# Kernel tuning notes

Hardware: AMD Instinct MI355X
Metric: run time of the kernel (lower is better)

## Reference

```python
import jax, jax.numpy as jnp
import numpy as np

N, E, H, NOISE, T, G = 50000, 400000, 128, 64, 128, 16
EPS = 1e-5


def _graph_norm(x, seg, num_seg, w, b, ms):
    # PyG GraphNorm: per-graph mean/std with learnable mean_scale
    cnt = jnp.maximum(jax.ops.segment_sum(jnp.ones((x.shape[0],), x.dtype), seg, num_segments=num_seg), 1.0)
    mean = jax.ops.segment_sum(x, seg, num_segments=num_seg) / cnt[:, None]
    out = x - mean[seg] * ms
    var = jax.ops.segment_sum(out * out, seg, num_segments=num_seg) / cnt[:, None]
    return w * out / jnp.sqrt(var + EPS)[seg] + b


def _forward(features, noise_mapping_emb, time_emb,
             We, be, Wp, bp, Wq, bq, Wr, br, Wu, bu, Wv, bv,
             gnh_w, gnh_b, gnh_ms, gne_w, gne_b, gne_ms,
             Wt, bt, ln_w, ln_b, Wo, bo,
             edge_mapping_idx, batch):
    src, dst = edge_mapping_idx[0], edge_mapping_idx[1]
    nme = noise_mapping_emb @ We + be                                  # [E,H]
    e_hat = nme @ Wp + bp + (features @ Wq + bq)[src] + (features @ Wr + br)[dst]
    gates = jax.nn.sigmoid(e_hat)
    aggr = jax.ops.segment_sum((features @ Wv + bv)[dst] * gates, src, num_segments=N)
    h = _graph_norm(features @ Wu + bu + aggr, batch, G, gnh_w, gnh_b, gnh_ms)
    eseg = batch[src]                                                  # edge -> graph
    e = _graph_norm(e_hat, eseg, G, gne_w, gne_b, gne_ms)
    h = jax.nn.relu(h)
    e = jax.nn.relu(e)
    e = e + (jax.nn.relu(time_emb) @ Wt + bt)[eseg]
    h = features + h
    # out_layer: LayerNorm -> SiLU -> Linear
    mu = jnp.mean(e, axis=-1, keepdims=True)
    var = jnp.mean((e - mu) ** 2, axis=-1, keepdims=True)
    ln = (e - mu) / jnp.sqrt(var + EPS) * ln_w + ln_b
    e = nme + jax.nn.silu(ln) @ Wo + bo
    return h, e


def setup_inputs() -> dict:
    key = jax.random.key(0)
    ks = jax.random.split(key, 16)

    def lin(k, i, o):
        k1, k2 = jax.random.split(k)
        s = 1.0 / np.sqrt(i)
        return (jax.random.uniform(k1, (i, o), minval=-s, maxval=s, dtype=jnp.float32),
                jax.random.uniform(k2, (o,), minval=-s, maxval=s, dtype=jnp.float32))

    We, be = lin(ks[5], NOISE, H)
    Wp, bp = lin(ks[6], H, H)
    Wq, bq = lin(ks[7], H, H)
    Wr, br = lin(ks[8], H, H)
    Wu, bu = lin(ks[9], H, H)
    Wv, bv = lin(ks[10], H, H)
    Wt, bt = lin(ks[11], T, H)
    Wo, bo = lin(ks[12], H, H)
    ones = jnp.ones((H,), jnp.float32)
    zeros = jnp.zeros((H,), jnp.float32)
    return dict(
        features=jax.random.normal(ks[0], (N, H), dtype=jnp.float32),
        edge_mapping_idx=jax.random.randint(ks[1], (2, E), 0, N),
        noise_mapping_emb=jax.random.normal(ks[2], (E, NOISE), dtype=jnp.float32),
        time_emb=jax.random.normal(ks[3], (G, T), dtype=jnp.float32),
        batch=jnp.sort(jax.random.randint(ks[4], (N,), 0, G)),
        We=We, be=be, Wp=Wp, bp=bp, Wq=Wq, bq=bq, Wr=Wr, br=br,
        Wu=Wu, bu=bu, Wv=Wv, bv=bv,
        gnh_w=ones, gnh_b=zeros, gnh_ms=ones,
        gne_w=ones, gne_b=zeros, gne_ms=ones,
        Wt=Wt, bt=bt, ln_w=ones, ln_b=zeros, Wo=Wo, bo=bo,
    )


def reference(features, edge_mapping_idx, noise_mapping_emb, time_emb, batch,
              We, be, Wp, bp, Wq, bq, Wr, br, Wu, bu, Wv, bv,
              gnh_w, gnh_b, gnh_ms, gne_w, gne_b, gne_ms,
              Wt, bt, ln_w, ln_b, Wo, bo):
    return _forward(features, noise_mapping_emb, time_emb,
                    We, be, Wp, bp, Wq, bq, Wr, br, Wu, bu, Wv, bv,
                    gnh_w, gnh_b, gnh_ms, gne_w, gne_b, gne_ms,
                    Wt, bt, ln_w, ln_b, Wo, bo,
                    edge_mapping_idx, batch)
```

## Files before the change

### kernel.cpp

```cpp
#include <hip/hip_runtime.h>

#define NN 50000
#define NE 400000
#define HD 128
#define ND 64
#define GG 16
#define EPSV 1e-5f
#define ETILE 64

#define SLEN (2 * GG * HD + GG)
#define PSTRIDE 4352
#define EP 512
#define HP 256
#define AGB 2048

typedef unsigned short u16;
typedef unsigned int   u32;
typedef unsigned char  u8;
typedef __attribute__((__ext_vector_type__(8))) __bf16 bf16x8;
typedef __attribute__((__ext_vector_type__(4))) float  f32x4;

__device__ __forceinline__ float us2f(u16 u) { return __uint_as_float(((u32)u) << 16); }
__device__ __forceinline__ u16 f2us(float f) {
    u32 u = __float_as_uint(f);
    u += 0x7fffu + ((u >> 16) & 1u);
    return (u16)(u >> 16);
}
__device__ __forceinline__ float sigmoidf_(float x) { return 1.f / (1.f + __expf(-x)); }

__global__ __launch_bounds__(256) void wep_kernel(
    const float* __restrict__ We, const float* __restrict__ Wp,
    const float* __restrict__ be, const float* __restrict__ bp,
    float* __restrict__ Wep, float* __restrict__ bep)
{
    __shared__ float wp[HD][HD];
    const int t = threadIdx.x;
    for (int i = t; i < HD * HD; i += 256) wp[i >> 7][i & 127] = Wp[i];
    __syncthreads();
    const int c = t & 127;
    for (int r = blockIdx.x * 4 + (t >> 7); r < (blockIdx.x + 1) * 4 && r < ND; r += 2) {
        float a = 0.f;
        for (int k = 0; k < HD; ++k) a = fmaf(We[r * HD + k], wp[k][c], a);
        Wep[r * HD + c] = a;
    }
    if (blockIdx.x == 0 && t < HD) {
        float a = bp[t];
        for (int k = 0; k < HD; ++k) a = fmaf(be[k], wp[k][t], a);
        bep[t] = a;
    }
}

__global__ __launch_bounds__(256) void prep_all_kernel(
    const float* __restrict__ Wq, const float* __restrict__ Wr,
    const float* __restrict__ Wv, const float* __restrict__ Wu,
    const float* __restrict__ Wo, const float* __restrict__ Wep,
    const float* __restrict__ We,
    u16* __restrict__ WqT, u16* __restrict__ WrT, u16* __restrict__ WvT,
    u16* __restrict__ WuT, u16* __restrict__ WoT, u16* __restrict__ WepT,
    u16* __restrict__ WeT)
{
    const float* in; u16* out; int K;
    switch (blockIdx.y) {
        case 0: in = Wq;  out = WqT;  K = HD; break;
        case 1: in = Wr;  out = WrT;  K = HD; break;
        case 2: in = Wv;  out = WvT;  K = HD; break;
        case 3: in = Wu;  out = WuT;  K = HD; break;
        case 4: in = Wo;  out = WoT;  K = HD; break;
        case 5: in = Wep; out = WepT; K = ND; break;
        default: in = We; out = WeT;  K = ND; break;
    }
    int idx = blockIdx.x * 256 + threadIdx.x;
    if (idx >= K * HD) return;
    int k = idx >> 7, n = idx & 127;
    out[n * K + k] = f2us(in[idx]);
}

__global__ __launch_bounds__(256) void hist_kernel(
    const int* __restrict__ srcArr, u32* __restrict__ deg)
{
    int e = blockIdx.x * 256 + threadIdx.x;
    if (e >= NE) return;
    atomicAdd(&deg[srcArr[e]], 1u);
}

#define SCAN_C 49
__global__ __launch_bounds__(1024) void scan_kernel(
    const u32* __restrict__ deg, int* __restrict__ start)
{
    __shared__ u32 sums[1024];
    const int t = threadIdx.x;
    const int i0 = t * SCAN_C;
    u32 tot = 0;
    for (int j = 0; j < SCAN_C; ++j) { int i = i0 + j; if (i < NN) tot += deg[i]; }
    sums[t] = tot;
    __syncthreads();
    for (int off = 1; off < 1024; off <<= 1) {
        u32 v = (t >= off) ? sums[t - off] : 0u;
        __syncthreads();
        sums[t] += v;
        __syncthreads();
    }
    u32 run = (t == 0) ? 0u : sums[t - 1];
    for (int j = 0; j < SCAN_C; ++j) {
        int i = i0 + j;
        if (i < NN) { start[i] = (int)run; run += deg[i]; }
    }
    if (t == 1023) start[NN] = (int)run;
}

__global__ __launch_bounds__(256) void scatter_kernel(
    const int* __restrict__ srcArr, const int* __restrict__ dstArr,
    const int* __restrict__ batch, const int* __restrict__ start,
    u32* __restrict__ cnt2, int* __restrict__ perm,
    int* __restrict__ iperm,
    int* __restrict__ src_csr, int* __restrict__ dst_csr,
    u8* __restrict__ g8csr)
{
    int e = blockIdx.x * 256 + threadIdx.x;
    if (e >= NE) return;
    int s = srcArr[e];
    u32 pos = atomicAdd(&cnt2[s], 1u);
    int j = start[s] + (int)pos;
    perm[j] = e;
    iperm[e] = j;
    src_csr[j] = s;
    dst_csr[j] = dstArr[e];
    g8csr[j] = (u8)batch[s];
}

__global__ __launch_bounds__(256) void proj4_kernel(
    const float* __restrict__ feat,
    const u16* __restrict__ WqT, const u16* __restrict__ WrT,
    const u16* __restrict__ WvT, const u16* __restrict__ WuT,
    const float* __restrict__ bq, const float* __restrict__ br,
    const float* __restrict__ bv, const float* __restrict__ bu,
    u16* __restrict__ fq, u16* __restrict__ fr, u16* __restrict__ fv,
    float* __restrict__ fu32)
{
    __shared__ __align__(16) u16 As[ETILE * HD];
    const int t = threadIdx.x;
    const int rbase = blockIdx.x * ETILE;
    #pragma unroll
    for (int i = 0; i < 16; ++i) {
        int idx2 = t + i * 256;
        int row = idx2 >> 6, p = idx2 & 63;
        int grow = rbase + row;
        float2 v = make_float2(0.f, 0.f);
        if (grow < NN) v = *reinterpret_cast<const float2*>(&feat[(size_t)grow * HD + p * 2]);
        u32 pk = (u32)f2us(v.x) | ((u32)f2us(v.y) << 16);
        int off = (row * 256 + p * 4) ^ ((row & 7) << 4);
        *reinterpret_cast<u32*>(reinterpret_cast<char*>(As) + off) = pk;
    }
    __syncthreads();
    const int w = t >> 6, lane = t & 63;
    const int rt = w * 16, l15 = lane & 15, kg = lane >> 4;
    const int lrow = rt + l15;
    bf16x8 afr[4];
    #pragma unroll
    for (int kk = 0; kk < 4; ++kk) {
        int off = (lrow * 256 + (kk * 32 + kg * 8) * 2) ^ ((lrow & 7) << 4);
        afr[kk] = *reinterpret_cast<const bf16x8*>(reinterpret_cast<const char*>(As) + off);
    }
    const u16* WTs[4] = {WqT, WrT, WvT, WuT};
    const float* Bs2[4] = {bq, br, bv, bu};
    u16* Os[3] = {fq, fr, fv};
    #pragma unroll
    for (int m = 0; m < 4; ++m) {
        f32x4 acc[8];
        #pragma unroll
        for (int nt = 0; nt < 8; ++nt) { acc[nt][0]=0.f; acc[nt][1]=0.f; acc[nt][2]=0.f; acc[nt][3]=0.f; }
        const u16* W = WTs[m];
        #pragma unroll
        for (int nt = 0; nt < 8; ++nt) {
            #pragma unroll
            for (int kk = 0; kk < 4; ++kk) {
                bf16x8 b = *reinterpret_cast<const bf16x8*>(&W[(nt * 16 + l15) * HD + kk * 32 + kg * 8]);
                acc[nt] = __builtin_amdgcn_mfma_f32_16x16x32_bf16(afr[kk], b, acc[nt], 0, 0, 0);
            }
        }
        #pragma unroll
        for (int nt = 0; nt < 8; ++nt) {
            int gcol = nt * 16 + l15;
            float bias = Bs2[m][gcol];
            #pragma unroll
            for (int i = 0; i < 4; ++i) {
                int grow = rbase + rt + kg * 4 + i;
                if (grow < NN) {
                    float v = acc[nt][i] + bias;
                    if (m < 3) Os[m][(size_t)grow * HD + gcol] = f2us(v);
                    else       fu32[(size_t)grow * HD + gcol] = v;
                }
            }
        }
    }
}

__global__ __launch_bounds__(256) void ehat_kernel(
    const float* __restrict__ noise, const u16* __restrict__ WepT,
    const float* __restrict__ bep,
    const u16* __restrict__ fq, const u16* __restrict__ fr,
    const int* __restrict__ perm, const int* __restrict__ src_csr,
    const int* __restrict__ dst_csr,
    u16* __restrict__ ehat_csr)
{
    __shared__ __align__(16) u16 WeL[1024 * 8];
    const int t = threadIdx.x;
    #pragma unroll
    for (int q = 0; q < 4; ++q) {
        int f = t + q * 256;
        int fl15 = f & 15, kgi = (f >> 4) & 7, fnt = f >> 7;
        *reinterpret_cast<uint4*>(&WeL[f * 8]) =
            *reinterpret_cast<const uint4*>(&WepT[(size_t)(fnt * 16 + fl15) * ND + kgi * 8]);
    }
    const int rbase = blockIdx.x * ETILE;
    const int w = t >> 6, lane = t & 63;
    const int rt = w * 16, l15 = lane & 15, kg = lane >> 4;
    const int jl = rbase + rt + l15;
    const int el = perm[jl];
    u32 an[2][4];
    #pragma unroll
    for (int kk = 0; kk < 2; ++kk) {
        const int c = kk * 32 + kg * 8;
        float4 n0 = *reinterpret_cast<const float4*>(&noise[(size_t)el * ND + c]);
        float4 n1 = *reinterpret_cast<const float4*>(&noise[(size_t)el * ND + c + 4]);
        an[kk][0] = (u32)f2us(n0.x) | ((u32)f2us(n0.y) << 16);
        an[kk][1] = (u32)f2us(n0.z) | ((u32)f2us(n0.w) << 16);
        an[kk][2] = (u32)f2us(n1.x) | ((u32)f2us(n1.y) << 16);
        an[kk][3] = (u32)f2us(n1.z) | ((u32)f2us(n1.w) << 16);
    }
    __syncthreads();
    f32x4 acc[8];
    #pragma unroll
    for (int nt = 0; nt < 8; ++nt) {
        float b = bep[nt * 16 + l15];
        acc[nt][0] = b; acc[nt][1] = b; acc[nt][2] = b; acc[nt][3] = b;
    }
    const int lid = kg * 16 + l15;
    #pragma unroll
    for (int nt = 0; nt < 8; ++nt) {
        #pragma unroll
        for (int kk = 0; kk < 2; ++kk) {
            bf16x8 b = *reinterpret_cast<const bf16x8*>(&WeL[(((nt * 2 + kk) * 64) + lid) * 8]);
            acc[nt] = __builtin_amdgcn_mfma_f32_16x16x32_bf16(
                *reinterpret_cast<const bf16x8*>(an[kk]), b, acc[nt], 0, 0, 0);
        }
    }
    #pragma unroll
    for (int i = 0; i < 4; ++i) {
        int jrow = rbase + rt + kg * 4 + i;
        int s = src_csr[jrow], d = dst_csr[jrow];
        #pragma unroll
        for (int nt = 0; nt < 8; ++nt) {
            int gcol = nt * 16 + l15;
            float v = acc[nt][i]
                    + us2f(fq[(size_t)s * HD + gcol]) + us2f(fr[(size_t)d * HD + gcol]);
            ehat_csr[(size_t)jrow * HD + gcol] = f2us(v);
        }
    }
}

__global__ __launch_bounds__(256) void aggr_kernel(
    const u16* __restrict__ ehat_csr, const u16* __restrict__ fv,
    const int* __restrict__ dst_csr, const int* __restrict__ start,
    float* __restrict__ xout)
{
    const int wid = blockIdx.x * 4 + (threadIdx.x >> 6);
    const int lane = threadIdx.x & 63;
    const int c0 = lane * 2;
    const int NW = AGB * 4;
    const int chunk = (NN + NW - 1) / NW;
    const int n0 = wid * chunk;
    const int n1 = min(NN, n0 + chunk);
    for (int node = n0; node < n1; ++node) {
        int s0 = start[node], s1 = start[node + 1];
        float2 uv = *reinterpret_cast<const float2*>(&xout[(size_t)node * HD + c0]);
        float a0 = 0.f, a1 = 0.f;
        for (int j = s0; j < s1; ++j) {
            int d = dst_csr[j];
            u32 ev = *reinterpret_cast<const u32*>(&ehat_csr[(size_t)j * HD + c0]);
            u32 vv = *reinterpret_cast<const u32*>(&fv[(size_t)d * HD + c0]);
            a0 = fmaf(sigmoidf_(us2f((u16)ev)),         us2f((u16)vv),         a0);
            a1 = fmaf(sigmoidf_(us2f((u16)(ev >> 16))), us2f((u16)(vv >> 16)), a1);
        }
        *reinterpret_cast<float2*>(&xout[(size_t)node * HD + c0]) =
            make_float2(a0 + uv.x, a1 + uv.y);
    }
}

__global__ __launch_bounds__(256) void hstats_part_kernel(
    const float* __restrict__ xout, const int* __restrict__ batch,
    float* __restrict__ hpart)
{
    __shared__ float sm[SLEN];
    const int t = threadIdx.x;
    for (int i = t; i < SLEN; i += 256) sm[i] = 0.f;
    __syncthreads();
    const int cg = t & 15, rq = t >> 4;
    const int c8 = cg * 8;
    const int chunk = (NN + HP - 1) / HP;
    const int rstart = blockIdx.x * chunk;
    const int rend = min(NN, rstart + chunk);
    float s0[8], z0[8];
    #pragma unroll
    for (int p = 0; p < 8; ++p) { s0[p] = 0.f; z0[p] = 0.f; }
    float cn = 0.f;
    int curg = -1;
    for (int row = rstart + rq; row < rend; row += 16) {
        int g = batch[row];
        if (g != curg) {
            if (curg >= 0) {
                #pragma unroll
                for (int p = 0; p < 8; ++p) {
                    unsafeAtomicAdd(&sm[curg * HD + c8 + p], s0[p]);
                    unsafeAtomicAdd(&sm[2048 + curg * HD + c8 + p], z0[p]);
                    s0[p] = 0.f; z0[p] = 0.f;
                }
                if (cg == 0) { unsafeAtomicAdd(&sm[4096 + curg], cn); }
                cn = 0.f;
            }
            curg = g;
        }
        float4 xa = *reinterpret_cast<const float4*>(&xout[(size_t)row * HD + c8]);
        float4 xb = *reinterpret_cast<const float4*>(&xout[(size_t)row * HD + c8 + 4]);
        const float xs8[8] = {xa.x, xa.y, xa.z, xa.w, xb.x, xb.y, xb.z, xb.w};
        #pragma unroll
        for (int p = 0; p < 8; ++p) { s0[p] += xs8[p]; z0[p] = fmaf(xs8[p], xs8[p], z0[p]); }
        cn += (cg == 0) ? 1.f : 0.f;
    }
    if (curg >= 0) {
        #pragma unroll
        for (int p = 0; p < 8; ++p) {
            unsafeAtomicAdd(&sm[curg * HD + c8 + p], s0[p]);
            unsafeAtomicAdd(&sm[2048 + curg * HD + c8 + p], z0[p]);
        }
        if (cg == 0) { unsafeAtomicAdd(&sm[4096 + curg], cn); }
    }
    __syncthreads();
    float* dst = hpart + (size_t)blockIdx.x * PSTRIDE;
    for (int i = t; i < SLEN; i += 256) dst[i] = sm[i];
}

__global__ __launch_bounds__(512) void estats_part_kernel(
    const u16* __restrict__ ehat_csr, const u8* __restrict__ g8csr,
    float* __restrict__ epart)
{
    __shared__ float sm[SLEN];
    const int t = threadIdx.x;
    for (int i = t; i < SLEN; i += 512) sm[i] = 0.f;
    __syncthreads();
    const int cg = t & 15, rq = t >> 4;
    const int c8 = cg * 8;
    const int chunk = (NE + EP - 1) / EP;
    const int rstart = blockIdx.x * chunk;
    const int rend = min(NE, rstart + chunk);
    float s0[8], z0[8];
    #pragma unroll
    for (int p = 0; p < 8; ++p) { s0[p] = 0.f; z0[p] = 0.f; }
    float cn = 0.f;
    int curg = -1;
    for (int row = rstart + rq; row < rend; row += 32) {
        int g = (int)g8csr[row];
        if (g != curg) {
            if (curg >= 0) {
                #pragma unroll
                for (int p = 0; p < 8; ++p) {
                    unsafeAtomicAdd(&sm[curg * HD + c8 + p], s0[p]);
                    unsafeAtomicAdd(&sm[2048 + curg * HD + c8 + p], z0[p]);
                    s0[p] = 0.f; z0[p] = 0.f;
                }
                if (cg == 0) { unsafeAtomicAdd(&sm[4096 + curg], cn); }
                cn = 0.f;
            }
            curg = g;
        }
        uint4 ev = *reinterpret_cast<const uint4*>(&ehat_csr[(size_t)row * HD + c8]);
        const u32 wds[4] = {ev.x, ev.y, ev.z, ev.w};
        #pragma unroll
        for (int p2 = 0; p2 < 4; ++p2) {
            float x0 = us2f((u16)wds[p2]);
            float x1 = us2f((u16)(wds[p2] >> 16));
            s0[2 * p2]     += x0; z0[2 * p2]     = fmaf(x0, x0, z0[2 * p2]);
            s0[2 * p2 + 1] += x1; z0[2 * p2 + 1] = fmaf(x1, x1, z0[2 * p2 + 1]);
        }
        cn += (cg == 0) ? 1.f : 0.f;
    }
    if (curg >= 0) {
        #pragma unroll
        for (int p = 0; p < 8; ++p) {
            unsafeAtomicAdd(&sm[curg * HD + c8 + p], s0[p]);
            unsafeAtomicAdd(&sm[2048 + curg * HD + c8 + p], z0[p]);
        }
        if (cg == 0) { unsafeAtomicAdd(&sm[4096 + curg], cn); }
    }
    __syncthreads();
    float* dst = epart + (size_t)blockIdx.x * PSTRIDE;
    for (int i = t; i < SLEN; i += 512) dst[i] = sm[i];
}

__global__ __launch_bounds__(256) void reduce_part_kernel(
    const float* __restrict__ part, int P, int csz, float* __restrict__ out)
{
    int j = blockIdx.x * 256 + threadIdx.x;
    if (j >= SLEN) return;
    int p0 = blockIdx.y * csz;
    int p1 = min(P, p0 + csz);
    float a = 0.f;
    for (int p = p0; p < p1; ++p) a += part[(size_t)p * PSTRIDE + j];
    out[(size_t)blockIdx.y * PSTRIDE + j] = a;
}

__global__ __launch_bounds__(256) void finstats_kernel(
    const float* __restrict__ statsH, const float* __restrict__ statsE,
    const float* __restrict__ gnh_ms, const float* __restrict__ gne_ms,
    const float* __restrict__ gnh_w, const float* __restrict__ gnh_b,
    const float* __restrict__ gne_w, const float* __restrict__ gne_b,
    const float* __restrict__ ln_w, const float* __restrict__ ln_b,
    const float* __restrict__ be, const float* __restrict__ bo,
    float* __restrict__ SBh, float* __restrict__ SBe,
    float* __restrict__ LNWB, float* __restrict__ bsum)
{
    const int t = threadIdx.x;
    if (t < 64) {
        LNWB[4 * t]     = ln_w[2 * t];
        LNWB[4 * t + 1] = ln_b[2 * t];
        LNWB[4 * t + 2] = ln_w[2 * t + 1];
        LNWB[4 * t + 3] = ln_b[2 * t + 1];
    }
    if (t >= 64 && t < 192) bsum[t - 64] = be[t - 64] + bo[t - 64];
    for (int i = t; i < GG * HD; i += 256) {
        int g = i >> 7, c = i & 127;
        {
            float cnt = fmaxf(statsH[4096 + g], 1.f);
            float mean = statsH[i] / cnt;
            float ex2 = statsH[2048 + i] / cnt;
            float off = mean * gnh_ms[c];
            float var = ex2 - 2.f * off * mean + off * off;
            float S = gnh_w[c] * rsqrtf(var + EPSV);
            SBh[2 * i]     = S;
            SBh[2 * i + 1] = gnh_b[c] - off * S;
        }
        {
            float cnt = fmaxf(statsE[4096 + g], 1.f);
            float mean = statsE[i] / cnt;
            float ex2 = statsE[2048 + i] / cnt;
            float off = mean * gne_ms[c];
            float var = ex2 - 2.f * off * mean + off * off;
            float S = gne_w[c] * rsqrtf(var + EPSV);
            SBe[2 * i]     = S;
            SBe[2 * i + 1] = gne_b[c] - off * S;
        }
    }
}

__global__ __launch_bounds__(256) void tproj_kernel(
    const float* __restrict__ time_emb, const float* __restrict__ Wt,
    const float* __restrict__ bt, float* __restrict__ tproj)
{
    __shared__ float te[GG][HD];
    const int t = threadIdx.x;
    for (int i = t; i < GG * HD; i += 256) te[i >> 7][i & 127] = fmaxf(time_emb[i], 0.f);
    __syncthreads();
    const int c = t & 127, rb = t >> 7;
    float acc[8];
    #pragma unroll
    for (int j = 0; j < 8; ++j) acc[j] = 0.f;
    for (int k = 0; k < HD; ++k) {
        float wv = Wt[k * HD + c];
        #pragma unroll
        for (int j = 0; j < 8; ++j) acc[j] = fmaf(te[rb + 2 * j][k], wv, acc[j]);
    }
    float b = bt[c];
    #pragma unroll
    for (int j = 0; j < 8; ++j) tproj[(rb + 2 * j) * HD + c] = acc[j] + b;
}

__global__ __launch_bounds__(256) void hfinal_kernel(
    const float* __restrict__ feat, const int* __restrict__ batch,
    const float* __restrict__ SBh, float* hout_x)
{
    int i = blockIdx.x * 256 + threadIdx.x;
    size_t base = (size_t)i * 4;
    if (base >= (size_t)NN * HD) return;
    int row = (int)(base >> 7), c0 = (int)(base & 127);
    int g = batch[row];
    float4 fe = *reinterpret_cast<const float4*>(&feat[base]);
    float4 xv = *reinterpret_cast<const float4*>(&hout_x[base]);
    float4 sb0 = *reinterpret_cast<const float4*>(&SBh[(size_t)(g * HD + c0) * 2]);
    float4 sb1 = *reinterpret_cast<const float4*>(&SBh[(size_t)(g * HD + c0 + 2) * 2]);
    float4 ou;
    ou.x = fe.x + fmaxf(fmaf(xv.x, sb0.x, sb0.y), 0.f);
    ou.y = fe.y + fmaxf(fmaf(xv.y, sb0.z, sb0.w), 0.f);
    ou.z = fe.z + fmaxf(fmaf(xv.z, sb1.x, sb1.y), 0.f);
    ou.w = fe.w + fmaxf(fmaf(xv.w, sb1.z, sb1.w), 0.f);
    *reinterpret_cast<float4*>(&hout_x[base]) = ou;
}

__global__ __launch_bounds__(256) void eprep_kernel(
    u16* __restrict__ ehat_csr, const u8* __restrict__ g8csr,
    const float* __restrict__ SBe, const float* __restrict__ tproj,
    const float* __restrict__ LNWB)
{
    const int t = threadIdx.x;
    const int lane = t & 63;
    const int cl = (lane & 15) * 8;
    const int wrow = (t >> 6) * 4 + (lane >> 4);
    for (int j = blockIdx.x * 16 + wrow; j < NE; j += gridDim.x * 16) {
        int g = g8csr[j];
        uint4 ev = *reinterpret_cast<const uint4*>(&ehat_csr[(size_t)j * HD + cl]);
        const u32 wds[4] = {ev.x, ev.y, ev.z, ev.w};
        float v[8];
        float lsum = 0.f;
        #pragma unroll
        for (int p = 0; p < 4; ++p) {
            int c2 = cl + p * 2;
            float x0 = us2f((u16)wds[p]);
            float x1 = us2f((u16)(wds[p] >> 16));
            float4 sb = *reinterpret_cast<const float4*>(&SBe[(size_t)(g * HD + c2) * 2]);
            float2 tp = *reinterpret_cast<const float2*>(&tproj[g * HD + c2]);
            float a0 = fmaxf(fmaf(x0, sb.x, sb.y), 0.f) + tp.x;
            float a1 = fmaxf(fmaf(x1, sb.z, sb.w), 0.f) + tp.y;
            v[p * 2] = a0; v[p * 2 + 1] = a1;
            lsum += a0 + a1;
        }
        lsum += __shfl_xor(lsum, 1, 64);
        lsum += __shfl_xor(lsum, 2, 64);
        lsum += __shfl_xor(lsum, 4, 64);
        lsum += __shfl_xor(lsum, 8, 64);
        float mu = lsum * (1.f / 128.f);
        float sq = 0.f;
        #pragma unroll
        for (int p = 0; p < 8; ++p) { float d = v[p] - mu; sq = fmaf(d, d, sq); }
        sq += __shfl_xor(sq, 1, 64);
        sq += __shfl_xor(sq, 2, 64);
        sq += __shfl_xor(sq, 4, 64);
        sq += __shfl_xor(sq, 8, 64);
        float rstd = rsqrtf(sq * (1.f / 128.f) + EPSV);
        u32 ow[4];
        #pragma unroll
        for (int p = 0; p < 4; ++p) {
            float4 lnwb = *reinterpret_cast<const float4*>(&LNWB[((cl >> 1) + p) * 4]);
            float l0 = (v[p * 2]     - mu) * rstd * lnwb.x + lnwb.y;
            float l1 = (v[p * 2 + 1] - mu) * rstd * lnwb.z + lnwb.w;
            float s0 = l0 * sigmoidf_(l0);
            float s1 = l1 * sigmoidf_(l1);
            ow[p] = (u32)f2us(s0) | ((u32)f2us(s1) << 16);
        }
        *reinterpret_cast<uint4*>(&ehat_csr[(size_t)j * HD + cl]) =
            make_uint4(ow[0], ow[1], ow[2], ow[3]);
    }
}

__global__ __launch_bounds__(512) void efinal_kernel(
    const u16* __restrict__ asilu, const float* __restrict__ noise,
    const int* __restrict__ iperm,
    const u16* __restrict__ WoT, const u16* __restrict__ WeT,
    const float* __restrict__ bsum,
    float* __restrict__ eout)
{
    __shared__ __align__(16) u16 WoL[2048 * 8];
    __shared__ __align__(16) u16 WeL[1024 * 8];
    const int t = threadIdx.x;
    #pragma unroll
    for (int q = 0; q < 4; ++q) {
        int f = t + q * 512;
        int l15 = f & 15, kgi = (f >> 4) & 15, nt = f >> 8;
        *reinterpret_cast<uint4*>(&WoL[f * 8]) =
            *reinterpret_cast<const uint4*>(&WoT[(size_t)(nt * 16 + l15) * HD + kgi * 8]);
    }
    #pragma unroll
    for (int q = 0; q < 2; ++q) {
        int f = t + q * 512;
        int l15 = f & 15, kgi = (f >> 4) & 7, nt = f >> 7;
        *reinterpret_cast<uint4*>(&WeL[f * 8]) =
            *reinterpret_cast<const uint4*>(&WeT[(size_t)(nt * 16 + l15) * ND + kgi * 8]);
    }

    const int rbase = blockIdx.x * 128;
    const int w = t >> 6, lane = t & 63;
    const int l15 = lane & 15, kg = lane >> 4;
    const int rt = w * 16;
    const int el = rbase + rt + l15;
    const int jl = iperm[el];

    bf16x8 aw[4];
    #pragma unroll
    for (int kk = 0; kk < 4; ++kk)
        aw[kk] = *reinterpret_cast<const bf16x8*>(&asilu[(size_t)jl * HD + kk * 32 + kg * 8]);
    u32 an[2][4];
    #pragma unroll
    for (int kk = 0; kk < 2; ++kk) {
        const int c = kk * 32 + kg * 8;
        float4 n0 = *reinterpret_cast<const float4*>(&noise[(size_t)el * ND + c]);
        float4 n1 = *reinterpret_cast<const float4*>(&noise[(size_t)el * ND + c + 4]);
        an[kk][0] = (u32)f2us(n0.x) | ((u32)f2us(n0.y) << 16);
        an[kk][1] = (u32)f2us(n0.z) | ((u32)f2us(n0.w) << 16);
        an[kk][2] = (u32)f2us(n1.x) | ((u32)f2us(n1.y) << 16);
        an[kk][3] = (u32)f2us(n1.z) | ((u32)f2us(n1.w) << 16);
    }
    __syncthreads();

    f32x4 acc[8];
    #pragma unroll
    for (int nt = 0; nt < 8; ++nt) {
        float bs = bsum[nt * 16 + l15];
        acc[nt][0] = bs; acc[nt][1] = bs; acc[nt][2] = bs; acc[nt][3] = bs;
    }
    const int lid = kg * 16 + l15;
    #pragma unroll
    for (int nt = 0; nt < 8; ++nt) {
        #pragma unroll
        for (int kk = 0; kk < 4; ++kk) {
            bf16x8 b = *reinterpret_cast<const bf16x8*>(&WoL[(((nt * 4 + kk) * 64) + lid) * 8]);
            acc[nt] = __builtin_amdgcn_mfma_f32_16x16x32_bf16(aw[kk], b, acc[nt], 0, 0, 0);
        }
        #pragma unroll
        for (int kk = 0; kk < 2; ++kk) {
            bf16x8 b = *reinterpret_cast<const bf16x8*>(&WeL[(((nt * 2 + kk) * 64) + lid) * 8]);
            acc[nt] = __builtin_amdgcn_mfma_f32_16x16x32_bf16(
                *reinterpret_cast<const bf16x8*>(an[kk]), b, acc[nt], 0, 0, 0);
        }
    }
    #pragma unroll
    for (int nt = 0; nt < 8; ++nt) {
        int gcol = nt * 16 + l15;
        #pragma unroll
        for (int i = 0; i < 4; ++i) {
            eout[(size_t)(rbase + rt + kg * 4 + i) * HD + gcol] = acc[nt][i];
        }
    }
}

extern "C" void kernel_launch(void* const* d_in, const int* in_sizes, int n_in,
                              void* d_out, int out_size, void* d_ws, size_t ws_size,
                              hipStream_t stream)
{
    const float* feat     = (const float*)d_in[0];
    const int*   eidx     = (const int*)d_in[1];
    const float* noise    = (const float*)d_in[2];
    const float* time_emb = (const float*)d_in[3];
    const int*   batch    = (const int*)d_in[4];
    const float* We = (const float*)d_in[5],  *be = (const float*)d_in[6];
    const float* Wp = (const float*)d_in[7],  *bp = (const float*)d_in[8];
    const float* Wq = (const float*)d_in[9],  *bq = (const float*)d_in[10];
    const float* Wr = (const float*)d_in[11], *br = (const float*)d_in[12];
    const float* Wu = (const float*)d_in[13], *bu = (const float*)d_in[14];
    const float* Wv = (const float*)d_in[15], *bv = (const float*)d_in[16];
    const float* gnh_w = (const float*)d_in[17], *gnh_b = (const float*)d_in[18], *gnh_ms = (const float*)d_in[19];
    const float* gne_w = (const float*)d_in[20], *gne_b = (const float*)d_in[21], *gne_ms = (const float*)d_in[22];
    const float* Wt = (const float*)d_in[23], *bt = (const float*)d_in[24];
    const float* ln_w = (const float*)d_in[25], *ln_b = (const float*)d_in[26];
    const float* Wo = (const float*)d_in[27], *bo = (const float*)d_in[28];

    const int* srcArr = eidx;
    const int* dstArr = eidx + NE;

    float* hout = (float*)d_out;
    float* eout = hout + (size_t)NN * HD;

    char* ws = (char*)d_ws;
    size_t off = 0;
    auto take = [&](size_t bytes) -> char* {
        char* p = ws + off;
        off = (off + bytes + 255) & ~(size_t)255;
        return p;
    };
    u16* ehat = (u16*)take((size_t)NE * HD * 2);
    u16* fq = (u16*)take((size_t)NN * HD * 2);
    u16* fr = (u16*)take((size_t)NN * HD * 2);
    u16* fv = (u16*)take((size_t)NN * HD * 2);
    u8*  g8csr = (u8*)take((size_t)NE);
    u32* deg  = (u32*)take((size_t)2 * NN * 4);
    u32* cnt2 = deg + NN;
    int* start = (int*)take((size_t)(NN + 1) * 4);
    int* perm  = (int*)take((size_t)NE * 4);
    int* iperm = (int*)take((size_t)NE * 4);
    int* src_csr = (int*)take((size_t)NE * 4);
    int* dst_csr = (int*)take((size_t)NE * 4);
    float* Wep = (float*)take((size_t)ND * HD * 4);
    float* bep = (float*)take((size_t)HD * 4);
    u16* WqT = (u16*)take((size_t)HD * HD * 2);
    u16* WrT = (u16*)take((size_t)HD * HD * 2);
    u16* WvT = (u16*)take((size_t)HD * HD * 2);
    u16* WuT = (u16*)take((size_t)HD * HD * 2);
    u16* WoT = (u16*)take((size_t)HD * HD * 2);
    u16* WepT = (u16*)take((size_t)HD * ND * 2);
    u16* WeT  = (u16*)take((size_t)HD * ND * 2);
    float* statsH = (float*)take((size_t)PSTRIDE * 4);
    float* statsE = (float*)take((size_t)PSTRIDE * 4);
    float* tproj  = (float*)take((size_t)GG * HD * 4);
    float* SBh    = (float*)take((size_t)GG * HD * 8);
    float* SBe    = (float*)take((size_t)GG * HD * 8);
    float* LNWB   = (float*)take((size_t)64 * 4 * 4);
    float* bsum   = (float*)take((size_t)HD * 4);
    float* epart  = (float*)take((size_t)EP * PSTRIDE * 4);
    float* hpart  = (float*)take((size_t)HP * PSTRIDE * 4);
    float* etmp   = (float*)take((size_t)8 * PSTRIDE * 4);
    float* htmp   = (float*)take((size_t)8 * PSTRIDE * 4);

    hipMemsetAsync(deg, 0, (size_t)2 * NN * 4, stream);

    wep_kernel<<<16, 256, 0, stream>>>(We, Wp, be, bp, Wep, bep);
    prep_all_kernel<<<dim3(64, 7), 256, 0, stream>>>(Wq, Wr, Wv, Wu, Wo, Wep, We,
                                                     WqT, WrT, WvT, WuT, WoT, WepT, WeT);
    hist_kernel<<<(NE + 255) / 256, 256, 0, stream>>>(srcArr, deg);
    scan_kernel<<<1, 1024, 0, stream>>>(deg, start);
    scatter_kernel<<<(NE + 255) / 256, 256, 0, stream>>>(srcArr, dstArr, batch, start,
                                                         cnt2, perm, iperm,
                                                         src_csr, dst_csr, g8csr);
    proj4_kernel<<<(NN + ETILE - 1) / ETILE, 256, 0, stream>>>(
        feat, WqT, WrT, WvT, WuT, bq, br, bv, bu, fq, fr, fv, hout);
    ehat_kernel<<<NE / ETILE, 256, 0, stream>>>(noise, WepT, bep, fq, fr,
                                                perm, src_csr, dst_csr, ehat);
    aggr_kernel<<<AGB, 256, 0, stream>>>(ehat, fv, dst_csr, start, hout);
    hstats_part_kernel<<<HP, 256, 0, stream>>>(hout, batch, hpart);
    estats_part_kernel<<<EP, 512, 0, stream>>>(ehat, g8csr, epart);
    {
        dim3 gA((SLEN + 255) / 256, 8);
        reduce_part_kernel<<<gA, 256, 0, stream>>>(hpart, HP, HP / 8, htmp);
        reduce_part_kernel<<<gA, 256, 0, stream>>>(epart, EP, EP / 8, etmp);
        dim3 gB((SLEN + 255) / 256, 1);
        reduce_part_kernel<<<gB, 256, 0, stream>>>(htmp, 8, 8, statsH);
        reduce_part_kernel<<<gB, 256, 0, stream>>>(etmp, 8, 8, statsE);
    }
    tproj_kernel<<<1, 256, 0, stream>>>(time_emb, Wt, bt, tproj);
    finstats_kernel<<<1, 256, 0, stream>>>(statsH, statsE, gnh_ms, gne_ms,
                                           gnh_w, gnh_b, gne_w, gne_b,
                                           ln_w, ln_b, be, bo,
                                           SBh, SBe, LNWB, bsum);
    eprep_kernel<<<2048, 256, 0, stream>>>(ehat, g8csr, SBe, tproj, LNWB);
    hfinal_kernel<<<(NN * HD / 4 + 255) / 256, 256, 0, stream>>>(feat, batch, SBh, hout);
    efinal_kernel<<<NE / 128, 512, 0, stream>>>(ehat, noise, iperm, WoT, WeT, bsum, eout);
}
```

Measured before the change: 692.0 us.

## Fuse node and edge GraphNorm statistics into the aggregation kernel

The aggregation kernel now also accumulates per-graph sum, sum-of-squares and count statistics for both the edge pre-activations and the aggregated node outputs, using shared-memory atomics on graph changes. This removes the two separate stats kernels, which each re-read ehat (E x H bf16) and the node output buffer. The cost is fewer blocks (512 x 512 threads) with more registers and shared memory in the aggregation pass, plus lower parallelism for the edge stats, which now follow the node-sharded CSR traversal. Edge graph ids come from batch[node], which is valid because edges are sorted by src.

Result: faster. 667.0 us (-3.6%).

```diff
diff --git a/kernel.cpp b/kernel.cpp
--- a/kernel.cpp
+++ b/kernel.cpp
@@ -10,9 +10,7 @@
 
 #define SLEN (2 * GG * HD + GG)
 #define PSTRIDE 4352
-#define EP 512
-#define HP 256
-#define AGB 2048
+#define ASB 512
 
 typedef unsigned short u16;
 typedef unsigned int   u32;
@@ -259,19 +257,48 @@
     }
 }
 
-__global__ __launch_bounds__(256) void aggr_kernel(
+__global__ __launch_bounds__(512) void aggr_stats_kernel(
     const u16* __restrict__ ehat_csr, const u16* __restrict__ fv,
     const int* __restrict__ dst_csr, const int* __restrict__ start,
-    float* __restrict__ xout)
-{
-    const int wid = blockIdx.x * 4 + (threadIdx.x >> 6);
-    const int lane = threadIdx.x & 63;
+    const int* __restrict__ batch, float* __restrict__ xout,
+    float* __restrict__ part)
+{
+    __shared__ float sm[2 * SLEN];
+    const int t = threadIdx.x;
+    for (int i = t; i < 2 * SLEN; i += 512) sm[i] = 0.f;
+    __syncthreads();
+    const int wid = blockIdx.x * 8 + (t >> 6);
+    const int lane = t & 63;
     const int c0 = lane * 2;
-    const int NW = AGB * 4;
+    const int NW = ASB * 8;
     const int chunk = (NN + NW - 1) / NW;
     const int n0 = wid * chunk;
     const int n1 = min(NN, n0 + chunk);
+    const float inc = (lane == 0) ? 1.f : 0.f;
+    float es0=0.f, es1=0.f, ez0=0.f, ez1=0.f, ecn=0.f;
+    float hs0=0.f, hs1=0.f, hz0=0.f, hz1=0.f, hcn=0.f;
+    int curg = -1;
     for (int node = n0; node < n1; ++node) {
+        int g = __builtin_amdgcn_readfirstlane(batch[node]);
+        if (g != curg) {
+            if (curg >= 0) {
+                unsafeAtomicAdd(&sm[curg * HD + c0],            es0);
+                unsafeAtomicAdd(&sm[curg * HD + c0 + 1],        es1);
+                unsafeAtomicAdd(&sm[2048 + curg * HD + c0],     ez0);
+                unsafeAtomicAdd(&sm[2048 + curg * HD + c0 + 1], ez1);
+                unsafeAtomicAdd(&sm[SLEN + curg * HD + c0],            hs0);
+                unsafeAtomicAdd(&sm[SLEN + curg * HD + c0 + 1],        hs1);
+                unsafeAtomicAdd(&sm[SLEN + 2048 + curg * HD + c0],     hz0);
+                unsafeAtomicAdd(&sm[SLEN + 2048 + curg * HD + c0 + 1], hz1);
+                if (lane == 0) {
+                    unsafeAtomicAdd(&sm[4096 + curg], ecn);
+                    unsafeAtomicAdd(&sm[SLEN + 4096 + curg], hcn);
+                }
+                es0=0.f; es1=0.f; ez0=0.f; ez1=0.f; ecn=0.f;
+                hs0=0.f; hs1=0.f; hz0=0.f; hz1=0.f; hcn=0.f;
+            }
+            curg = g;
+        }
         int s0 = start[node], s1 = start[node + 1];
         float2 uv = *reinterpret_cast<const float2*>(&xout[(size_t)node * HD + c0]);
         float a0 = 0.f, a1 = 0.f;
@@ -279,133 +306,51 @@
             int d = dst_csr[j];
             u32 ev = *reinterpret_cast<const u32*>(&ehat_csr[(size_t)j * HD + c0]);
             u32 vv = *reinterpret_cast<const u32*>(&fv[(size_t)d * HD + c0]);
-            a0 = fmaf(sigmoidf_(us2f((u16)ev)),         us2f((u16)vv),         a0);
-            a1 = fmaf(sigmoidf_(us2f((u16)(ev >> 16))), us2f((u16)(vv >> 16)), a1);
-        }
-        *reinterpret_cast<float2*>(&xout[(size_t)node * HD + c0]) =
-            make_float2(a0 + uv.x, a1 + uv.y);
-    }
-}
-
-__global__ __launch_bounds__(256) void hstats_part_kernel(
-    const float* __restrict__ xout, const int* __restrict__ batch,
-    float* __restrict__ hpart)
-{
-    __shared__ float sm[SLEN];
-    const int t = threadIdx.x;
-    for (int i = t; i < SLEN; i += 256) sm[i] = 0.f;
-    __syncthreads();
-    const int cg = t & 15, rq = t >> 4;
-    const int c8 = cg * 8;
-    const int chunk = (NN + HP - 1) / HP;
-    const int rstart = blockIdx.x * chunk;
-    const int rend = min(NN, rstart + chunk);
-    float s0[8], z0[8];
-    #pragma unroll
-    for (int p = 0; p < 8; ++p) { s0[p] = 0.f; z0[p] = 0.f; }
-    float cn = 0.f;
-    int curg = -1;
-    for (int row = rstart + rq; row < rend; row += 16) {
-        int g = batch[row];
-        if (g != curg) {
-            if (curg >= 0) {
-                #pragma unroll
-                for (int p = 0; p < 8; ++p) {
-                    unsafeAtomicAdd(&sm[curg * HD + c8 + p], s0[p]);
-                    unsafeAtomicAdd(&sm[2048 + curg * HD + c8 + p], z0[p]);
-                    s0[p] = 0.f; z0[p] = 0.f;
-                }
-                if (cg == 0) { unsafeAtomicAdd(&sm[4096 + curg], cn); }
-                cn = 0.f;
-            }
-            curg = g;
-        }
-        float4 xa = *reinterpret_cast<const float4*>(&xout[(size_t)row * HD + c8]);
-        float4 xb = *reinterpret_cast<const float4*>(&xout[(size_t)row * HD + c8 + 4]);
-        const float xs8[8] = {xa.x, xa.y, xa.z, xa.w, xb.x, xb.y, xb.z, xb.w};
-        #pragma unroll
-        for (int p = 0; p < 8; ++p) { s0[p] += xs8[p]; z0[p] = fmaf(xs8[p], xs8[p], z0[p]); }
-        cn += (cg == 0) ? 1.f : 0.f;
+            float x0 = us2f((u16)ev), x1 = us2f((u16)(ev >> 16));
+            a0 = fmaf(sigmoidf_(x0), us2f((u16)vv),         a0);
+            a1 = fmaf(sigmoidf_(x1), us2f((u16)(vv >> 16)), a1);
+            es0 += x0; ez0 = fmaf(x0, x0, ez0);
+            es1 += x1; ez1 = fmaf(x1, x1, ez1);
+            ecn += inc;
+        }
+        float xx0 = a0 + uv.x, xx1 = a1 + uv.y;
+        *reinterpret_cast<float2*>(&xout[(size_t)node * HD + c0]) = make_float2(xx0, xx1);
+        hs0 += xx0; hz0 = fmaf(xx0, xx0, hz0);
+        hs1 += xx1; hz1 = fmaf(xx1, xx1, hz1);
+        hcn += inc;
     }
     if (curg >= 0) {
-        #pragma unroll
-        for (int p = 0; p < 8; ++p) {
-            unsafeAtomicAdd(&sm[curg * HD + c8 + p], s0[p]);
-            unsafeAtomicAdd(&sm[2048 + curg * HD + c8 + p], z0[p]);
-        }
-        if (cg == 0) { unsafeAtomicAdd(&sm[4096 + curg], cn); }
-    }
-    __syncthreads();
-    float* dst = hpart + (size_t)blockIdx.x * PSTRIDE;
-    for (int i = t; i < SLEN; i += 256) dst[i] = sm[i];
-}
-
-__global__ __launch_bounds__(512) void estats_part_kernel(
-    const u16* __restrict__ ehat_csr, const u8* __restrict__ g8csr,
-    float* __restrict__ epart)
-{
-    __shared__ float sm[SLEN];
-    const int t = threadIdx.x;
-    for (int i = t; i < SLEN; i += 512) sm[i] = 0.f;
-    __syncthreads();
-    const int cg = t & 15, rq = t >> 4;
-    const int c8 = cg * 8;
-    const int chunk = (NE + EP - 1) / EP;
-    const int rstart = blockIdx.x * chunk;
-    const int rend = min(NE, rstart + chunk);
-    float s0[8], z0[8];
-    #pragma unroll
-    for (int p = 0; p < 8; ++p) { s0[p] = 0.f; z0[p] = 0.f; }
-    float cn = 0.f;
-    int curg = -1;
-    for (int row = rstart + rq; row < rend; row += 32) {
-        int g = (int)g8csr[row];
-        if (g != curg) {
-            if (curg >= 0) {
-                #pragma unroll
-                for (int p = 0; p < 8; ++p) {
-                    unsafeAtomicAdd(&sm[curg * HD + c8 + p], s0[p]);
-                    unsafeAtomicAdd(&sm[2048 + curg * HD + c8 + p], z0[p]);
-                    s0[p] = 0.f; z0[p] = 0.f;
-                }
-                if (cg == 0) { unsafeAtomicAdd(&sm[4096 + curg], cn); }
-                cn = 0.f;
-            }
-            curg = g;
-        }
-        uint4 ev = *reinterpret_cast<const uint4*>(&ehat_csr[(size_t)row * HD + c8]);
-        const u32 wds[4] = {ev.x, ev.y, ev.z, ev.w};
-        #pragma unroll
-        for (int p2 = 0; p2 < 4; ++p2) {
-            float x0 = us2f((u16)wds[p2]);
-            float x1 = us2f((u16)(wds[p2] >> 16));
-            s0[2 * p2]     += x0; z0[2 * p2]     = fmaf(x0, x0, z0[2 * p2]);
-            s0[2 * p2 + 1] += x1; z0[2 * p2 + 1] = fmaf(x1, x1, z0[2 * p2 + 1]);
-        }
-        cn += (cg == 0) ? 1.f : 0.f;
-    }
-    if (curg >= 0) {
-        #pragma unroll
-        for (int p = 0; p < 8; ++p) {
-            unsafeAtomicAdd(&sm[curg * HD + c8 + p], s0[p]);
-            unsafeAtomicAdd(&sm[2048 + curg * HD + c8 + p], z0[p]);
-        }
-        if (cg == 0) { unsafeAtomicAdd(&sm[4096 + curg], cn); }
-    }
-    __syncthreads();
-    float* dst = epart + (size_t)blockIdx.x * PSTRIDE;
-    for (int i = t; i < SLEN; i += 512) dst[i] = sm[i];
+        unsafeAtomicAdd(&sm[curg * HD + c0],            es0);
+        unsafeAtomicAdd(&sm[curg * HD + c0 + 1],        es1);
+        unsafeAtomicAdd(&sm[2048 + curg * HD + c0],     ez0);
+        unsafeAtomicAdd(&sm[2048 + curg * HD + c0 + 1], ez1);
+        unsafeAtomicAdd(&sm[SLEN + curg * HD + c0],            hs0);
+        unsafeAtomicAdd(&sm[SLEN + curg * HD + c0 + 1],        hs1);
+        unsafeAtomicAdd(&sm[SLEN + 2048 + curg * HD + c0],     hz0);
+        unsafeAtomicAdd(&sm[SLEN + 2048 + curg * HD + c0 + 1], hz1);
+        if (lane == 0) {
+            unsafeAtomicAdd(&sm[4096 + curg], ecn);
+            unsafeAtomicAdd(&sm[SLEN + 4096 + curg], hcn);
+        }
+    }
+    __syncthreads();
+    float* dst = part + (size_t)blockIdx.x * (2 * PSTRIDE);
+    for (int i = t; i < SLEN; i += 512) {
+        dst[i] = sm[i];
+        dst[PSTRIDE + i] = sm[SLEN + i];
+    }
 }
 
 __global__ __launch_bounds__(256) void reduce_part_kernel(
-    const float* __restrict__ part, int P, int csz, float* __restrict__ out)
+    const float* __restrict__ part, int P, int csz, int instride,
+    float* __restrict__ out)
 {
     int j = blockIdx.x * 256 + threadIdx.x;
     if (j >= SLEN) return;
     int p0 = blockIdx.y * csz;
     int p1 = min(P, p0 + csz);
     float a = 0.f;
-    for (int p = p0; p < p1; ++p) a += part[(size_t)p * PSTRIDE + j];
+    for (int p = p0; p < p1; ++p) a += part[(size_t)p * instride + j];
     out[(size_t)blockIdx.y * PSTRIDE + j] = a;
 }
 
@@ -563,16 +508,16 @@
     #pragma unroll
     for (int q = 0; q < 4; ++q) {
         int f = t + q * 512;
-        int l15 = f & 15, kgi = (f >> 4) & 15, nt = f >> 8;
+        int fl15 = f & 15, kgi = (f >> 4) & 15, fnt = f >> 8;
         *reinterpret_cast<uint4*>(&WoL[f * 8]) =
-            *reinterpret_cast<const uint4*>(&WoT[(size_t)(nt * 16 + l15) * HD + kgi * 8]);
+            *reinterpret_cast<const uint4*>(&WoT[(size_t)(fnt * 16 + fl15) * HD + kgi * 8]);
     }
     #pragma unroll
     for (int q = 0; q < 2; ++q) {
         int f = t + q * 512;
-        int l15 = f & 15, kgi = (f >> 4) & 7, nt = f >> 7;
+        int fl15 = f & 15, kgi = (f >> 4) & 7, fnt = f >> 7;
         *reinterpret_cast<uint4*>(&WeL[f * 8]) =
-            *reinterpret_cast<const uint4*>(&WeT[(size_t)(nt * 16 + l15) * ND + kgi * 8]);
+            *reinterpret_cast<const uint4*>(&WeT[(size_t)(fnt * 16 + fl15) * ND + kgi * 8]);
     }
 
     const int rbase = blockIdx.x * 128;
@@ -692,8 +637,7 @@
     float* SBe    = (float*)take((size_t)GG * HD * 8);
     float* LNWB   = (float*)take((size_t)64 * 4 * 4);
     float* bsum   = (float*)take((size_t)HD * 4);
-    float* epart  = (float*)take((size_t)EP * PSTRIDE * 4);
-    float* hpart  = (float*)take((size_t)HP * PSTRIDE * 4);
+    float* part   = (float*)take((size_t)ASB * 2 * PSTRIDE * 4);
     float* etmp   = (float*)take((size_t)8 * PSTRIDE * 4);
     float* htmp   = (float*)take((size_t)8 * PSTRIDE * 4);
 
@@ -711,16 +655,14 @@
         feat, WqT, WrT, WvT, WuT, bq, br, bv, bu, fq, fr, fv, hout);
     ehat_kernel<<<NE / ETILE, 256, 0, stream>>>(noise, WepT, bep, fq, fr,
                                                 perm, src_csr, dst_csr, ehat);
-    aggr_kernel<<<AGB, 256, 0, stream>>>(ehat, fv, dst_csr, start, hout);
-    hstats_part_kernel<<<HP, 256, 0, stream>>>(hout, batch, hpart);
-    estats_part_kernel<<<EP, 512, 0, stream>>>(ehat, g8csr, epart);
+    aggr_stats_kernel<<<ASB, 512, 0, stream>>>(ehat, fv, dst_csr, start, batch, hout, part);
     {
         dim3 gA((SLEN + 255) / 256, 8);
-        reduce_part_kernel<<<gA, 256, 0, stream>>>(hpart, HP, HP / 8, htmp);
-        reduce_part_kernel<<<gA, 256, 0, stream>>>(epart, EP, EP / 8, etmp);
+        reduce_part_kernel<<<gA, 256, 0, stream>>>(part, ASB, ASB / 8, 2 * PSTRIDE, etmp);
+        reduce_part_kernel<<<gA, 256, 0, stream>>>(part + PSTRIDE, ASB, ASB / 8, 2 * PSTRIDE, htmp);
         dim3 gB((SLEN + 255) / 256, 1);
-        reduce_part_kernel<<<gB, 256, 0, stream>>>(htmp, 8, 8, statsH);
-        reduce_part_kernel<<<gB, 256, 0, stream>>>(etmp, 8, 8, statsE);
+        reduce_part_kernel<<<gB, 256, 0, stream>>>(etmp, 8, 8, PSTRIDE, statsE);
+        reduce_part_kernel<<<gB, 256, 0, stream>>>(htmp, 8, 8, PSTRIDE, statsH);
     }
     tproj_kernel<<<1, 256, 0, stream>>>(time_emb, Wt, bt, tproj);
     finstats_kernel<<<1, 256, 0, stream>>>(statsH, statsE, gnh_ms, gne_ms,
```
